# Performance work log

Hardware: AMD Instinct MI355X
Metric: run time of the kernel (lower is better)

Reference implementation:

```python
import jax, jax.numpy as jnp
import numpy as np

S = 3      # num_subset
CI = 64    # inter_channels
C = 256    # in_channels == out_channels
T = 400    # num_frame
V = 25     # num_node


def make_pe(channel, joint_num, time_len, domain):
    if domain == 'temporal':
        pos = np.repeat(np.arange(time_len), joint_num).astype(np.float32)
    else:
        pos = np.tile(np.arange(joint_num), time_len).astype(np.float32)
    pe = np.zeros((time_len * joint_num, channel), dtype=np.float32)
    div = np.exp(np.arange(0, channel, 2, dtype=np.float32) * (-np.log(10000.0) / channel))
    pe[:, 0::2] = np.sin(pos[:, None] * div[None, :])
    pe[:, 1::2] = np.cos(pos[:, None] * div[None, :])
    pe = pe.reshape(time_len, joint_num, channel).transpose(2, 0, 1)[None]  # (1,C,T,V)
    return jnp.asarray(pe)


def setup_inputs() -> dict:
    key = jax.random.key(0)
    ks = jax.random.split(key, 10)
    def w(k, shape):
        return jax.random.normal(k, shape, jnp.float32) * 0.02
    return {
        'x': jax.random.normal(ks[0], (4, C, T, V), jnp.float32),
        'x1': jax.random.normal(ks[1], (4, C, T, V), jnp.float32),
        'pe_s': make_pe(C, V, T, 'spatial'),
        'pe_t': make_pe(C, V, T, 'temporal'),
        'in_nets_W': w(ks[2], (2 * S * CI, C)), 'in_nets_b': jnp.zeros((2 * S * CI,), jnp.float32),
        'alphas': jnp.ones((1, S, 1, 1), jnp.float32),
        'attention0s': jnp.ones((1, S, V, V), jnp.float32) / V,
        'out_nets_W': w(ks[3], (C, S * C)), 'out_nets_b': jnp.zeros((C,), jnp.float32),
        'out_nets_g': jnp.ones((C,), jnp.float32), 'out_nets_beta': jnp.zeros((C,), jnp.float32),
        'ff_nets_W': w(ks[4], (C, C)), 'ff_nets_b': jnp.zeros((C,), jnp.float32),
        'ff_nets_g': jnp.ones((C,), jnp.float32), 'ff_nets_beta': jnp.zeros((C,), jnp.float32),
        'in_nett_W': w(ks[5], (2 * S * CI, C)), 'in_nett_b': jnp.zeros((2 * S * CI,), jnp.float32),
        'alphat': jnp.ones((1, S, 1, 1), jnp.float32),
        'attention0t': jnp.broadcast_to(jnp.eye(T, dtype=jnp.float32), (1, S, T, T)),
        'out_nett_W': w(ks[6], (C, S * C)), 'out_nett_b': jnp.zeros((C,), jnp.float32),
        'out_nett_g': jnp.ones((C,), jnp.float32), 'out_nett_beta': jnp.zeros((C,), jnp.float32),
        'ff_nett_W': w(ks[7], (C, C)), 'ff_nett_b': jnp.zeros((C,), jnp.float32),
        'ff_nett_g': jnp.ones((C,), jnp.float32), 'ff_nett_beta': jnp.zeros((C,), jnp.float32),
        'case': 0,
    }


def _conv1x1(W, b, x):
    return jnp.einsum('oc,nctv->notv', W, x) + b[None, :, None, None]

def _bn(x, g, b):  # eval-mode BN (running mean 0, var 1) -> channel affine
    return x * g[None, :, None, None] + b[None, :, None, None]

def _lrelu(x):
    return jnp.where(x >= 0, x, 0.1 * x)


def reference(x, x1, pe_s, pe_t, in_nets_W, in_nets_b, alphas, attention0s,
              out_nets_W, out_nets_b, out_nets_g, out_nets_beta,
              ff_nets_W, ff_nets_b, ff_nets_g, ff_nets_beta,
              in_nett_W, in_nett_b, alphat, attention0t,
              out_nett_W, out_nett_b, out_nett_g, out_nett_beta,
              ff_nett_W, ff_nett_b, ff_nett_g, ff_nett_beta, case):
    # case == 0 path of the original forward (dropout p=0 -> identity).
    def spatial(xi):
        y = xi + pe_s  # spatial positional encoding
        def half(xh, yh):  # xh, yh: (2, C, T, V) half-batch, as in x.view(2,2,C,T,V)
            qk = _conv1x1(in_nets_W, in_nets_b, yh).reshape(2, 2 * S, CI, T, V)
            q, k = qk[:, :S], qk[:, S:]
            att = jnp.tanh(jnp.einsum('nsctu,nsctv->nsuv', q, k) / (CI * T)) * alphas + attention0s
            return jnp.einsum('nctv,nsvw->nsctw', xh, att).reshape(2, S * C, T, V)
        z = jnp.concatenate([half(xi[:2], y[:2]), half(xi[2:], y[2:])], axis=0)
        h = _lrelu(xi + _bn(_conv1x1(out_nets_W, out_nets_b, z), out_nets_g, out_nets_beta))
        return _lrelu(xi + _bn(_conv1x1(ff_nets_W, ff_nets_b, h), ff_nets_g, ff_nets_beta))

    def temporal(yi):
        z = yi + pe_t  # temporal positional encoding
        def half(yh, zh):
            qk = _conv1x1(in_nett_W, in_nett_b, zh).reshape(2, 2 * S, CI, T, V)
            q, k = qk[:, :S], qk[:, S:]
            att = jnp.tanh(jnp.einsum('nsctv,nscqv->nstq', q, k) / (CI * V)) * alphat + attention0t
            return jnp.einsum('nctv,nstq->nscqv', yh, att).reshape(2, S * C, T, V)
        z2 = jnp.concatenate([half(yi[:2], z[:2]), half(yi[2:], z[2:])], axis=0)
        h = _lrelu(yi + _bn(_conv1x1(out_nett_W, out_nett_b, z2), out_nett_g, out_nett_beta))
        return _lrelu(yi + _bn(_conv1x1(ff_nett_W, ff_nett_b, h), ff_nett_g, ff_nett_beta))

    out0 = temporal(spatial(x))
    out1 = temporal(spatial(x1))
    return jnp.stack([out0, out1], axis=0)  # (2, 4, C, T, V)
```

## Files before the change

### kernel.cpp

```cpp
#include <hip/hip_runtime.h>
#include <math.h>


#define PP 10000
#define SAMP 2560000

typedef __attribute__((ext_vector_type(8))) __bf16 bf16x8;
typedef __attribute__((ext_vector_type(4))) float f32x4;

#define LIDX(g, r)  ((g) * 128 + ((r) ^ (g)))
#define LIDXB(g, r) ((g) * 64 + ((r) ^ (g)))

__device__ __forceinline__ float4 ld4(const float* p) { return *(const float4*)p; }
__device__ __forceinline__ float lrelu(float v) { return v >= 0.f ? v : 0.1f * v; }

template<int MODE, bool PE, bool BGLOB, bool OUTGLOB>
__global__ __launch_bounds__(256)
void gemm_mfma(const float* __restrict__ W, int Kw,
               const float* __restrict__ bias,
               const float* __restrict__ g, const float* __restrict__ beta,
               const float* __restrict__ bg0, const float* __restrict__ bg1,
               const float* __restrict__ bw,
               const float* __restrict__ pe,
               const float* rg0, const float* rg1,
               float* out, int n0, int M, int K)
{
    const int ln = blockIdx.z;
    const int ns = n0 + ln;
    const int p0 = blockIdx.x * 64;
    const int m0 = blockIdx.y * 128;
    const int tid = threadIdx.x;

    const float* Bp;
    if (BGLOB)
        Bp = (ns < 4) ? bg0 + (size_t)ns * (size_t)K * PP
                      : bg1 + (size_t)(ns - 4) * (size_t)K * PP;
    else
        Bp = bw + (size_t)ln * (size_t)K * PP;

    __shared__ __align__(16) bf16x8 AhL[512];
    __shared__ __align__(16) bf16x8 AlL[512];
    __shared__ __align__(16) bf16x8 BhL[256];
    __shared__ __align__(16) bf16x8 BlL[256];

    const int am  = tid >> 1;
    const int akb = (tid & 1) * 16;
    const int ag0 = akb >> 3;
    const float* wrow = W + (size_t)(m0 + am) * Kw + akb;

    const int bp  = tid & 63;
    const int bg_ = tid >> 6;
    const int bkg = bg_ * 8;
    const int gp  = p0 + bp;
    const bool pok = gp < PP;

    const int lane = tid & 63;
    const int wv = tid >> 6;
    const int wr = (wv >> 1) * 64, wc = (wv & 1) * 32;
    const int lr = lane & 15;
    const int lg = lane >> 4;

    f32x4 acc[4][2];
#pragma unroll
    for (int i = 0; i < 4; i++)
#pragma unroll
        for (int j = 0; j < 2; j++) acc[i][j] = (f32x4){0.f, 0.f, 0.f, 0.f};

    float4 wreg[4];
    float  breg[8];

    auto loadAB = [&](int kc) {
#pragma unroll
        for (int q = 0; q < 4; q++) wreg[q] = ld4(wrow + kc + q * 4);
        const int kk = kc + bkg;
#pragma unroll
        for (int i = 0; i < 8; i++) {
            float v = 0.f;
            if (pok) {
                v = Bp[(size_t)(kk + i) * PP + gp];
                if (PE) v += pe[(size_t)(kk + i) * PP + gp];
            }
            breg[i] = v;
        }
    };

    loadAB(0);

    for (int k0 = 0; k0 < K; k0 += 32) {
        {
            bf16x8 h0, h1, l0, l1;
#pragma unroll
            for (int q = 0; q < 4; q++) {
                const float vs0 = wreg[q].x, vs1 = wreg[q].y, vs2 = wreg[q].z, vs3 = wreg[q].w;
                __bf16 hh; const int ib = q * 4;
#define CVTA(c, val) { hh = (__bf16)(val); __bf16 ll = (__bf16)((val) - (float)hh); \
    if (ib + c < 8) { h0[ib + c] = hh; l0[ib + c] = ll; } else { h1[ib + c - 8] = hh; l1[ib + c - 8] = ll; } }
                CVTA(0, vs0) CVTA(1, vs1) CVTA(2, vs2) CVTA(3, vs3)
#undef CVTA
            }
            AhL[LIDX(ag0, am)]     = h0;
            AhL[LIDX(ag0 + 1, am)] = h1;
            AlL[LIDX(ag0, am)]     = l0;
            AlL[LIDX(ag0 + 1, am)] = l1;
        }
        {
            bf16x8 hb, lb;
#pragma unroll
            for (int i = 0; i < 8; i++) {
                __bf16 hh = (__bf16)breg[i];
                hb[i] = hh;
                lb[i] = (__bf16)(breg[i] - (float)hh);
            }
            BhL[LIDXB(bg_, bp)] = hb;
            BlL[LIDXB(bg_, bp)] = lb;
        }
        __syncthreads();

        const int kn = k0 + 32;
        if (kn < K) loadAB(kn);

        bf16x8 fbh[2], fbl[2];
#pragma unroll
        for (int fj = 0; fj < 2; fj++) {
            fbh[fj] = BhL[LIDXB(lg, wc + fj * 16 + lr)];
            fbl[fj] = BlL[LIDXB(lg, wc + fj * 16 + lr)];
        }
#pragma unroll
        for (int fi = 0; fi < 4; fi++) {
            bf16x8 fah = AhL[LIDX(lg, wr + fi * 16 + lr)];
            bf16x8 fal = AlL[LIDX(lg, wr + fi * 16 + lr)];
#pragma unroll
            for (int fj = 0; fj < 2; fj++) {
                acc[fi][fj] = __builtin_amdgcn_mfma_f32_16x16x32_bf16(fah, fbh[fj], acc[fi][fj], 0, 0, 0);
                acc[fi][fj] = __builtin_amdgcn_mfma_f32_16x16x32_bf16(fah, fbl[fj], acc[fi][fj], 0, 0, 0);
                acc[fi][fj] = __builtin_amdgcn_mfma_f32_16x16x32_bf16(fal, fbh[fj], acc[fi][fj], 0, 0, 0);
            }
        }
        __syncthreads();
    }

    const int rb = (lane >> 4) * 4;

    if (MODE == 5) {
#pragma unroll
        for (int fi = 0; fi < 4; fi++) {
            const int mb = m0 + wr + fi * 16 + rb;
            const int sec = mb >> 6, cl = mb & 63;
            float* qt = out + (size_t)ln * 3840000ull + (size_t)sec * 640000ull + cl;
            const float b0 = bias[mb], b1 = bias[mb + 1], b2 = bias[mb + 2], b3 = bias[mb + 3];
#pragma unroll
            for (int fj = 0; fj < 2; fj++) {
                const int p = p0 + wc + fj * 16 + lr;
                if (p >= PP) continue;
                const int t = p / 25, v = p - t * 25;
                f32x4 a = acc[fi][fj];
                *(float4*)(qt + (size_t)t * 1600 + v * 64) =
                    make_float4(a[0] + b0, a[1] + b1, a[2] + b2, a[3] + b3);
            }
        }
        return;
    }

    float* op = out + (OUTGLOB ? (size_t)ns : (size_t)ln) * (size_t)M * PP;
    const float* resp = nullptr;
    if (MODE == 1 || MODE == 4)
        resp = (ns < 4) ? rg0 + (size_t)ns * SAMP : rg1 + (size_t)(ns - 4) * SAMP;

#pragma unroll
    for (int fi = 0; fi < 4; fi++) {
#pragma unroll
        for (int r = 0; r < 4; r++) {
            const int m = m0 + wr + fi * 16 + rb + r;
            const float bi = (MODE == 0 || MODE == 1 || MODE == 4) ? bias[m] : 0.f;
            const float gi = (MODE == 1 || MODE == 4) ? g[m] : 0.f;
            const float be = (MODE == 1 || MODE == 4) ? beta[m] : 0.f;
            const size_t rowoff = (size_t)m * PP;
#pragma unroll
            for (int fj = 0; fj < 2; fj++) {
                const int p = p0 + wc + fj * 16 + lr;
                if (p >= PP) continue;
                const float a = acc[fi][fj][r];
                float val;
                if (MODE == 0)      val = a + bi;
                else if (MODE == 2) val = a;
                else if (MODE == 3) val = op[rowoff + p] + a;
                else if (MODE == 4) val = lrelu(resp[rowoff + p] + gi * (op[rowoff + p] + a + bi) + be);
                else                val = lrelu(resp[rowoff + p] + gi * (a + bi) + be);
                op[rowoff + p] = val;
            }
        }
    }
}

__global__ __launch_bounds__(256)
void apply_t_mfma(const float* __restrict__ y, const float* __restrict__ attT,
                  float* __restrict__ z, int n0, int s)
{
    const int ln = blockIdx.z;
    const int ns = n0 + ln;
    const int j0 = blockIdx.x * 64;
    const int q0 = blockIdx.y * 128;
    const float* A = attT + ((size_t)ln * 3 + s) * 160000ull;
    const float* Y = y + (size_t)ns * SAMP;
    float* zout = z + (size_t)ln * SAMP;
    const int tid = threadIdx.x;

    __shared__ __align__(16) bf16x8 AhL[512];
    __shared__ __align__(16) bf16x8 AlL[512];
    __shared__ __align__(16) bf16x8 BhL[256];
    __shared__ __align__(16) bf16x8 BlL[256];

    const int am  = tid >> 1;
    const int akb = (tid & 1) * 16;
    const int ag0 = akb >> 3;
    const int qA  = q0 + am;
    const float* arow = A + (size_t)qA * 400;

    const int bp  = tid & 63;
    const int bg_ = tid >> 6;
    const int bkg = bg_ * 8;
    const int j   = j0 + bp;
    const int cB  = j / 25, vB = j % 25;
    const float* yrow = Y + (size_t)cB * PP + vB;

    const int lane = tid & 63;
    const int wv = tid >> 6;
    const int wr = (wv >> 1) * 64, wc = (wv & 1) * 32;
    const int lr = lane & 15;
    const int lg = lane >> 4;

    f32x4 acc[4][2];
#pragma unroll
    for (int i = 0; i < 4; i++)
#pragma unroll
        for (int jj = 0; jj < 2; jj++) acc[i][jj] = (f32x4){0.f, 0.f, 0.f, 0.f};

    float4 wreg[4];
    float  breg[8];

    auto loadAB = [&](int kc) {
#pragma unroll
        for (int q = 0; q < 4; q++) {
            const int ks_ = kc + akb + q * 4;
            float4 v = make_float4(0.f, 0.f, 0.f, 0.f);
            if (qA < 400 && ks_ < 400) v = ld4(arow + ks_);
            wreg[q] = v;
        }
        const int kb = kc + bkg;
#pragma unroll
        for (int i = 0; i < 8; i++) {
            const int t = kb + i;
            breg[i] = (t < 400) ? yrow[(size_t)t * 25] : 0.f;
        }
    };

    loadAB(0);

    for (int k0 = 0; k0 < 416; k0 += 32) {
        {
            bf16x8 h0, h1, l0, l1;
#pragma unroll
            for (int q = 0; q < 4; q++) {
                const float vs0 = wreg[q].x, vs1 = wreg[q].y, vs2 = wreg[q].z, vs3 = wreg[q].w;
                __bf16 hh; const int ib = q * 4;
#define CVTA(c, val) { hh = (__bf16)(val); __bf16 ll = (__bf16)((val) - (float)hh); \
    if (ib + c < 8) { h0[ib + c] = hh; l0[ib + c] = ll; } else { h1[ib + c - 8] = hh; l1[ib + c - 8] = ll; } }
                CVTA(0, vs0) CVTA(1, vs1) CVTA(2, vs2) CVTA(3, vs3)
#undef CVTA
            }
            AhL[LIDX(ag0, am)]     = h0;
            AhL[LIDX(ag0 + 1, am)] = h1;
            AlL[LIDX(ag0, am)]     = l0;
            AlL[LIDX(ag0 + 1, am)] = l1;
        }
        {
            bf16x8 hb, lb;
#pragma unroll
            for (int i = 0; i < 8; i++) {
                __bf16 hh = (__bf16)breg[i];
                hb[i] = hh;
                lb[i] = (__bf16)(breg[i] - (float)hh);
            }
            BhL[LIDXB(bg_, bp)] = hb;
            BlL[LIDXB(bg_, bp)] = lb;
        }
        __syncthreads();

        const int kn = k0 + 32;
        if (kn < 416) loadAB(kn);

        bf16x8 fbh[2], fbl[2];
#pragma unroll
        for (int fj = 0; fj < 2; fj++) {
            fbh[fj] = BhL[LIDXB(lg, wc + fj * 16 + lr)];
            fbl[fj] = BlL[LIDXB(lg, wc + fj * 16 + lr)];
        }
#pragma unroll
        for (int fi = 0; fi < 4; fi++) {
            bf16x8 fah = AhL[LIDX(lg, wr + fi * 16 + lr)];
            bf16x8 fal = AlL[LIDX(lg, wr + fi * 16 + lr)];
#pragma unroll
            for (int fj = 0; fj < 2; fj++) {
                acc[fi][fj] = __builtin_amdgcn_mfma_f32_16x16x32_bf16(fah, fbh[fj], acc[fi][fj], 0, 0, 0);
                acc[fi][fj] = __builtin_amdgcn_mfma_f32_16x16x32_bf16(fah, fbl[fj], acc[fi][fj], 0, 0, 0);
                acc[fi][fj] = __builtin_amdgcn_mfma_f32_16x16x32_bf16(fal, fbh[fj], acc[fi][fj], 0, 0, 0);
            }
        }
        __syncthreads();
    }

    const int rb = (lane >> 4) * 4;
#pragma unroll
    for (int fi = 0; fi < 4; fi++) {
#pragma unroll
        for (int r = 0; r < 4; r++) {
            const int q = q0 + wr + fi * 16 + rb + r;
            if (q >= 400) continue;
#pragma unroll
            for (int fj = 0; fj < 2; fj++) {
                const int p = j0 + wc + fj * 16 + lr;
                const int c = p / 25, v = p - c * 25;
                zout[(size_t)c * PP + (size_t)q * 25 + v] = acc[fi][fj][r];
            }
        }
    }
}

__global__ __launch_bounds__(256)
void scores_t_mfma(const float* __restrict__ qkT,
                   const float* __restrict__ alphat,
                   const float* __restrict__ att0t,
                   float* __restrict__ aT)
{
    const int idx = blockIdx.y;
    const int s = idx % 3, ln = idx / 3;
    const int t0 = (blockIdx.x % 7) * 64;
    const int q0 = (blockIdx.x / 7) * 128;
    const float* base = qkT + (size_t)ln * 3840000ull;
    const float* Aq = base + (size_t)(3 + s) * 640000ull;
    const float* Bt = base + (size_t)s * 640000ull;
    const int tid = threadIdx.x;

    __shared__ __align__(16) bf16x8 AhL[512];
    __shared__ __align__(16) bf16x8 AlL[512];
    __shared__ __align__(16) bf16x8 BhL[256];
    __shared__ __align__(16) bf16x8 BlL[256];

    const int am  = tid >> 1;
    const int akb = (tid & 1) * 16;
    const int ag0 = akb >> 3;
    const int qA  = q0 + am;
    const float* arow = Aq + (size_t)qA * 1600 + akb;
    const bool aok = qA < 400;

    const int bp  = tid & 63;
    const int bg_ = tid >> 6;
    const int bkg = bg_ * 8;
    const int tB  = t0 + bp;
    const float* brow = Bt + (size_t)tB * 1600 + bkg;
    const bool bok = tB < 400;

    const int lane = tid & 63;
    const int wv = tid >> 6;
    const int wr = (wv >> 1) * 64, wc = (wv & 1) * 32;
    const int lr = lane & 15;
    const int lg = lane >> 4;

    f32x4 acc[4][2];
#pragma unroll
    for (int i = 0; i < 4; i++)
#pragma unroll
        for (int j = 0; j < 2; j++) acc[i][j] = (f32x4){0.f, 0.f, 0.f, 0.f};

    float4 areg[4];
    float4 brg[2];

    auto loadAB = [&](int kc) {
#pragma unroll
        for (int q = 0; q < 4; q++)
            areg[q] = aok ? ld4(arow + kc + q * 4) : make_float4(0.f, 0.f, 0.f, 0.f);
        brg[0] = bok ? ld4(brow + kc)     : make_float4(0.f, 0.f, 0.f, 0.f);
        brg[1] = bok ? ld4(brow + kc + 4) : make_float4(0.f, 0.f, 0.f, 0.f);
    };

    loadAB(0);

    for (int k0 = 0; k0 < 1600; k0 += 32) {
        {
            bf16x8 h0, h1, l0, l1;
#pragma unroll
            for (int q = 0; q < 4; q++) {
                const float vs0 = areg[q].x, vs1 = areg[q].y, vs2 = areg[q].z, vs3 = areg[q].w;
                __bf16 hh; const int ib = q * 4;
#define CVTA(c, val) { hh = (__bf16)(val); __bf16 ll = (__bf16)((val) - (float)hh); \
    if (ib + c < 8) { h0[ib + c] = hh; l0[ib + c] = ll; } else { h1[ib + c - 8] = hh; l1[ib + c - 8] = ll; } }
                CVTA(0, vs0) CVTA(1, vs1) CVTA(2, vs2) CVTA(3, vs3)
#undef CVTA
            }
            AhL[LIDX(ag0, am)]     = h0;
            AhL[LIDX(ag0 + 1, am)] = h1;
            AlL[LIDX(ag0, am)]     = l0;
            AlL[LIDX(ag0 + 1, am)] = l1;
        }
        {
            bf16x8 hb, lb;
#pragma unroll
            for (int e = 0; e < 2; e++) {
                const float v0 = (e ? brg[1].x : brg[0].x), v1 = (e ? brg[1].y : brg[0].y);
                const float v2 = (e ? brg[1].z : brg[0].z), v3 = (e ? brg[1].w : brg[0].w);
                __bf16 hh;
#define CVTB(c, val) { hh = (__bf16)(val); hb[e * 4 + c] = hh; lb[e * 4 + c] = (__bf16)((val) - (float)hh); }
                CVTB(0, v0) CVTB(1, v1) CVTB(2, v2) CVTB(3, v3)
#undef CVTB
            }
            BhL[LIDXB(bg_, bp)] = hb;
            BlL[LIDXB(bg_, bp)] = lb;
        }
        __syncthreads();

        const int kn = k0 + 32;
        if (kn < 1600) loadAB(kn);

        bf16x8 fbh[2], fbl[2];
#pragma unroll
        for (int fj = 0; fj < 2; fj++) {
            fbh[fj] = BhL[LIDXB(lg, wc + fj * 16 + lr)];
            fbl[fj] = BlL[LIDXB(lg, wc + fj * 16 + lr)];
        }
#pragma unroll
        for (int fi = 0; fi < 4; fi++) {
            bf16x8 fah = AhL[LIDX(lg, wr + fi * 16 + lr)];
            bf16x8 fal = AlL[LIDX(lg, wr + fi * 16 + lr)];
#pragma unroll
            for (int fj = 0; fj < 2; fj++) {
                acc[fi][fj] = __builtin_amdgcn_mfma_f32_16x16x32_bf16(fah, fbh[fj], acc[fi][fj], 0, 0, 0);
                acc[fi][fj] = __builtin_amdgcn_mfma_f32_16x16x32_bf16(fah, fbl[fj], acc[fi][fj], 0, 0, 0);
                acc[fi][fj] = __builtin_amdgcn_mfma_f32_16x16x32_bf16(fal, fbh[fj], acc[fi][fj], 0, 0, 0);
            }
        }
        __syncthreads();
    }

    const int rb = (lane >> 4) * 4;
    const float al = alphat[s];
    float* aTp = aT + (size_t)idx * 160000ull;
    const float* a0p = att0t + (size_t)s * 160000ull;

#pragma unroll
    for (int fi = 0; fi < 4; fi++) {
        const int qb = q0 + wr + fi * 16 + rb;
#pragma unroll
        for (int fj = 0; fj < 2; fj++) {
            const int t = t0 + wc + fj * 16 + lr;
            if (t >= 400) continue;
#pragma unroll
            for (int r = 0; r < 4; r++) {
                const int q = qb + r;
                if (q >= 400) continue;
                aTp[(size_t)q * 400 + t] =
                    tanhf(acc[fi][fj][r] * (1.f / 1600.f)) * al + a0p[(size_t)t * 400 + q];
            }
        }
    }
}

__global__ __launch_bounds__(256)
void scores_s_partial(const float* __restrict__ qk, float* __restrict__ part)
{
    const int chunk = blockIdx.x, s = blockIdx.y, ln = blockIdx.z;
    const float* qsec = qk + ((size_t)ln * 384 + s * 64) * PP + (size_t)chunk * 3200;
    const float* ksec = qk + ((size_t)ln * 384 + (3 + s) * 64) * PP + (size_t)chunk * 3200;
    __shared__ float QL[3200];
    __shared__ float KL[3200];
    const int tid = threadIdx.x;
    for (int i = tid; i < 3200; i += 256) {
        QL[i] = qsec[i];
        KL[i] = ksec[i];
    }
    __syncthreads();
    const int o0 = tid, o1 = tid + 256, o2 = tid + 512;
    const int u0 = o0 / 25, v0 = o0 % 25;
    const int u1 = o1 / 25, v1 = o1 % 25;
    const int u2 = o2 / 25, v2 = o2 % 25;
    float a0 = 0.f, a1 = 0.f, a2 = 0.f;
#pragma unroll 8
    for (int r = 0; r < 128; r++) {
        int ro = r * 25;
        a0 = fmaf(QL[ro + u0], KL[ro + v0], a0);
        a1 = fmaf(QL[ro + u1], KL[ro + v1], a1);
        if (tid < 113) a2 = fmaf(QL[ro + u2], KL[ro + v2], a2);
    }
    float* pp = part + (((size_t)(ln * 3 + s)) * 200 + chunk) * 625;
    pp[o0] = a0;
    pp[o1] = a1;
    if (tid < 113) pp[o2] = a2;
}

__global__ void scores_s_final(const float* __restrict__ part,
                               const float* __restrict__ alphas,
                               const float* __restrict__ att0s,
                               float* __restrict__ atts)
{
    const int idx = blockIdx.x;
    const int s = idx % 3;
    const int o = threadIdx.x;
    if (o >= 625) return;
    const float* pb = part + (size_t)idx * 200 * 625 + o;
    float sum = 0.f;
#pragma unroll 8
    for (int i = 0; i < 200; i++) sum += pb[(size_t)i * 625];
    atts[(size_t)idx * 625 + o] = tanhf(sum * (1.f / 25600.f)) * alphas[s] + att0s[s * 625 + o];
}

__global__ __launch_bounds__(256)
void apply_s_kernel(const float* __restrict__ x0, const float* __restrict__ x1,
                    const float* __restrict__ atts, float* __restrict__ z,
                    int n0, int s)
{
    const int ln = blockIdx.y;
    const int ns = n0 + ln;
    const int tid = threadIdx.x;
    __shared__ float attL[700];
    for (int i = tid; i < 700; i += 256) attL[i] = 0.f;
    __syncthreads();
    for (int i = tid; i < 625; i += 256) {
        int v = i / 25, w = i % 25;
        attL[v * 28 + w] = atts[(size_t)ln * 1875 + s * 625 + i];
    }
    __syncthreads();
    const float* xp = (ns < 4) ? x0 + (size_t)ns * SAMP : x1 + (size_t)(ns - 4) * SAMP;
    const int r0 = (blockIdx.x * 256 + tid) * 2;
    const float* xr0 = xp + (size_t)r0 * 25;
    float xr[2][25];
#pragma unroll
    for (int i = 0; i < 2; i++)
#pragma unroll
        for (int v = 0; v < 25; v++) xr[i][v] = xr0[i * 25 + v];
    const int c0 = r0 / 400, t0 = r0 % 400;

    float4 acc0[7], acc1[7];
#pragma unroll
    for (int w4 = 0; w4 < 7; w4++) {
        acc0[w4] = make_float4(0.f, 0.f, 0.f, 0.f);
        acc1[w4] = make_float4(0.f, 0.f, 0.f, 0.f);
    }
#pragma unroll
    for (int v = 0; v < 25; v++) {
        const float4* arow = (const float4*)&attL[v * 28];
        float xv0 = xr[0][v], xv1 = xr[1][v];
#pragma unroll
        for (int w4 = 0; w4 < 7; w4++) {
            float4 a = arow[w4];
            acc0[w4].x = fmaf(xv0, a.x, acc0[w4].x);
            acc0[w4].y = fmaf(xv0, a.y, acc0[w4].y);
            acc0[w4].z = fmaf(xv0, a.z, acc0[w4].z);
            acc0[w4].w = fmaf(xv0, a.w, acc0[w4].w);
            acc1[w4].x = fmaf(xv1, a.x, acc1[w4].x);
            acc1[w4].y = fmaf(xv1, a.y, acc1[w4].y);
            acc1[w4].z = fmaf(xv1, a.z, acc1[w4].z);
            acc1[w4].w = fmaf(xv1, a.w, acc1[w4].w);
        }
    }
    float* zp = z + (size_t)ln * SAMP + (size_t)c0 * PP + (size_t)t0 * 25;
#pragma unroll
    for (int w4 = 0; w4 < 7; w4++) {
        int wb = w4 * 4;
        if (wb + 0 < 25) zp[wb + 0] = acc0[w4].x;
        if (wb + 1 < 25) zp[wb + 1] = acc0[w4].y;
        if (wb + 2 < 25) zp[wb + 2] = acc0[w4].z;
        if (wb + 3 < 25) zp[wb + 3] = acc0[w4].w;
    }
#pragma unroll
    for (int w4 = 0; w4 < 7; w4++) {
        int wb = w4 * 4;
        if (wb + 0 < 25) zp[25 + wb + 0] = acc1[w4].x;
        if (wb + 1 < 25) zp[25 + wb + 1] = acc1[w4].y;
        if (wb + 2 < 25) zp[25 + wb + 2] = acc1[w4].z;
        if (wb + 3 < 25) zp[25 + wb + 3] = acc1[w4].w;
    }
}

extern "C" void kernel_launch(void* const* d_in, const int* in_sizes, int n_in,
                              void* d_out, int out_size, void* d_ws, size_t ws_size,
                              hipStream_t stream)
{
    const float* x    = (const float*)d_in[0];
    const float* x1   = (const float*)d_in[1];
    const float* pe_s = (const float*)d_in[2];
    const float* pe_t = (const float*)d_in[3];
    const float* Wsi  = (const float*)d_in[4];
    const float* bsi  = (const float*)d_in[5];
    const float* alphas = (const float*)d_in[6];
    const float* att0s  = (const float*)d_in[7];
    const float* Wso  = (const float*)d_in[8];
    const float* bso  = (const float*)d_in[9];
    const float* gso  = (const float*)d_in[10];
    const float* beso = (const float*)d_in[11];
    const float* Wsf  = (const float*)d_in[12];
    const float* bsf  = (const float*)d_in[13];
    const float* gsf  = (const float*)d_in[14];
    const float* besf = (const float*)d_in[15];
    const float* Wti  = (const float*)d_in[16];
    const float* bti  = (const float*)d_in[17];
    const float* alphat = (const float*)d_in[18];
    const float* att0t  = (const float*)d_in[19];
    const float* Wto  = (const float*)d_in[20];
    const float* bto  = (const float*)d_in[21];
    const float* gto  = (const float*)d_in[22];
    const float* beto = (const float*)d_in[23];
    const float* Wtf  = (const float*)d_in[24];
    const float* btf  = (const float*)d_in[25];
    const float* gtf  = (const float*)d_in[26];
    const float* betf = (const float*)d_in[27];

    float* outp = (float*)d_out;
    const float* outpB = outp + 4ull * SAMP;

    int G = 1;
    for (int g = 8; g >= 1; g >>= 1) {
        if ((size_t)g * 27587500ull <= ws_size) { G = g; break; }
    }

    float* A   = (float*)d_ws;
    float* Zs  = A  + (size_t)G * 3840000ull;
    float* aT  = Zs + (size_t)G * 2560000ull;
    float* sp  = aT + (size_t)G * 480000ull;
    float* as  = sp + (size_t)G * 15000ull;

    dim3 blk(256);
    for (int n0 = 0; n0 < 8; n0 += G) {
        dim3 gIn(157, 3, G), gOut(157, 2, G);

        gemm_mfma<0, true, true, false><<<gIn, blk, 0, stream>>>(
            Wsi, 256, bsi, nullptr, nullptr, x, x1, nullptr, pe_s,
            nullptr, nullptr, A, n0, 384, 256);
        scores_s_partial<<<dim3(200, 3, G), blk, 0, stream>>>(A, Zs);
        scores_s_final<<<dim3(3 * G), dim3(640), 0, stream>>>(Zs, alphas, att0s, as);
        for (int s = 0; s < 3; s++) {
            apply_s_kernel<<<dim3(200, G), blk, 0, stream>>>(x, x1, as, Zs, n0, s);
            if (s == 0)
                gemm_mfma<2, false, false, false><<<gOut, blk, 0, stream>>>(
                    Wso + s * 256, 768, nullptr, nullptr, nullptr, nullptr, nullptr, Zs,
                    nullptr, nullptr, nullptr, A, n0, 256, 256);
            else if (s == 1)
                gemm_mfma<3, false, false, false><<<gOut, blk, 0, stream>>>(
                    Wso + s * 256, 768, nullptr, nullptr, nullptr, nullptr, nullptr, Zs,
                    nullptr, nullptr, nullptr, A, n0, 256, 256);
            else
                gemm_mfma<4, false, false, false><<<gOut, blk, 0, stream>>>(
                    Wso + s * 256, 768, bso, gso, beso, nullptr, nullptr, Zs,
                    nullptr, x, x1, A, n0, 256, 256);
        }
        gemm_mfma<1, false, false, true><<<gOut, blk, 0, stream>>>(
            Wsf, 256, bsf, gsf, besf, nullptr, nullptr, A, nullptr,
            x, x1, outp, n0, 256, 256);

        gemm_mfma<5, true, true, false><<<gIn, blk, 0, stream>>>(
            Wti, 256, bti, nullptr, nullptr, outp, outpB, nullptr, pe_t,
            nullptr, nullptr, A, n0, 384, 256);
        scores_t_mfma<<<dim3(28, 3 * G), blk, 0, stream>>>(A, alphat, att0t, aT);
        for (int s = 0; s < 3; s++) {
            apply_t_mfma<<<dim3(100, 4, G), blk, 0, stream>>>(outp, aT, Zs, n0, s);
            if (s == 0)
                gemm_mfma<2, false, false, false><<<gOut, blk, 0, stream>>>(
                    Wto + s * 256, 768, nullptr, nullptr, nullptr, nullptr, nullptr, Zs,
                    nullptr, nullptr, nullptr, A, n0, 256, 256);
            else if (s == 1)
                gemm_mfma<3, false, false, false><<<gOut, blk, 0, stream>>>(
                    Wto + s * 256, 768, nullptr, nullptr, nullptr, nullptr, nullptr, Zs,
                    nullptr, nullptr, nullptr, A, n0, 256, 256);
            else
                gemm_mfma<4, false, false, false><<<gOut, blk, 0, stream>>>(
                    Wto + s * 256, 768, bto, gto, beto, nullptr, nullptr, Zs,
                    nullptr, outp, outpB, A, n0, 256, 256);
        }
        gemm_mfma<1, false, false, true><<<gOut, blk, 0, stream>>>(
            Wtf, 256, btf, gtf, betf, nullptr, nullptr, A, nullptr,
            outp, outpB, outp, n0, 256, 256);
    }
}
```

Baseline: 1.812 ms.

## Merge per-subset output GEMMs into one K=768 GEMM over stacked Z buffers

Apply kernels now write each subset's result into its own slice of a tripled Z workspace. A single output-projection GEMM with K=768 then runs with the fused BN/residual/lrelu epilogue. This replaces three K=256 GEMMs that read-modify-wrote partial sums through global memory. The cost is a larger workspace per sample, which may reduce the batch group size G if the workspace is limited.

```diff
diff --git a/kernel.cpp b/kernel.cpp
--- a/kernel.cpp
+++ b/kernel.cpp
@@ -163,7 +163,7 @@
 
     float* op = out + (OUTGLOB ? (size_t)ns : (size_t)ln) * (size_t)M * PP;
     const float* resp = nullptr;
-    if (MODE == 1 || MODE == 4)
+    if (MODE == 1)
         resp = (ns < 4) ? rg0 + (size_t)ns * SAMP : rg1 + (size_t)(ns - 4) * SAMP;
 
 #pragma unroll
@@ -171,9 +171,9 @@
 #pragma unroll
         for (int r = 0; r < 4; r++) {
             const int m = m0 + wr + fi * 16 + rb + r;
-            const float bi = (MODE == 0 || MODE == 1 || MODE == 4) ? bias[m] : 0.f;
-            const float gi = (MODE == 1 || MODE == 4) ? g[m] : 0.f;
-            const float be = (MODE == 1 || MODE == 4) ? beta[m] : 0.f;
+            const float bi = (MODE == 0 || MODE == 1) ? bias[m] : 0.f;
+            const float gi = (MODE == 1) ? g[m] : 0.f;
+            const float be = (MODE == 1) ? beta[m] : 0.f;
             const size_t rowoff = (size_t)m * PP;
 #pragma unroll
             for (int fj = 0; fj < 2; fj++) {
@@ -181,11 +181,8 @@
                 if (p >= PP) continue;
                 const float a = acc[fi][fj][r];
                 float val;
-                if (MODE == 0)      val = a + bi;
-                else if (MODE == 2) val = a;
-                else if (MODE == 3) val = op[rowoff + p] + a;
-                else if (MODE == 4) val = lrelu(resp[rowoff + p] + gi * (op[rowoff + p] + a + bi) + be);
-                else                val = lrelu(resp[rowoff + p] + gi * (a + bi) + be);
+                if (MODE == 0) val = a + bi;
+                else           val = lrelu(resp[rowoff + p] + gi * (a + bi) + be);
                 op[rowoff + p] = val;
             }
         }
@@ -202,7 +199,7 @@
     const int q0 = blockIdx.y * 128;
     const float* A = attT + ((size_t)ln * 3 + s) * 160000ull;
     const float* Y = y + (size_t)ns * SAMP;
-    float* zout = z + (size_t)ln * SAMP;
+    float* zout = z + ((size_t)ln * 3 + s) * SAMP;
     const int tid = threadIdx.x;
 
     __shared__ __align__(16) bf16x8 AhL[512];
@@ -561,7 +558,7 @@
             acc1[w4].w = fmaf(xv1, a.w, acc1[w4].w);
         }
     }
-    float* zp = z + (size_t)ln * SAMP + (size_t)c0 * PP + (size_t)t0 * 25;
+    float* zp = z + ((size_t)ln * 3 + s) * SAMP + (size_t)c0 * PP + (size_t)t0 * 25;
 #pragma unroll
     for (int w4 = 0; w4 < 7; w4++) {
         int wb = w4 * 4;
@@ -618,14 +615,13 @@
 
     int G = 1;
     for (int g = 8; g >= 1; g >>= 1) {
-        if ((size_t)g * 27587500ull <= ws_size) { G = g; break; }
+        if ((size_t)g * 48007500ull <= ws_size) { G = g; break; }
     }
 
     float* A   = (float*)d_ws;
     float* Zs  = A  + (size_t)G * 3840000ull;
-    float* aT  = Zs + (size_t)G * 2560000ull;
-    float* sp  = aT + (size_t)G * 480000ull;
-    float* as  = sp + (size_t)G * 15000ull;
+    float* aT  = Zs + (size_t)G * 7680000ull;
+    float* as  = aT + (size_t)G * 480000ull;
 
     dim3 blk(256);
     for (int n0 = 0; n0 < 8; n0 += G) {
@@ -636,21 +632,11 @@
             nullptr, nullptr, A, n0, 384, 256);
         scores_s_partial<<<dim3(200, 3, G), blk, 0, stream>>>(A, Zs);
         scores_s_final<<<dim3(3 * G), dim3(640), 0, stream>>>(Zs, alphas, att0s, as);
-        for (int s = 0; s < 3; s++) {
+        for (int s = 0; s < 3; s++)
             apply_s_kernel<<<dim3(200, G), blk, 0, stream>>>(x, x1, as, Zs, n0, s);
-            if (s == 0)
-                gemm_mfma<2, false, false, false><<<gOut, blk, 0, stream>>>(
-                    Wso + s * 256, 768, nullptr, nullptr, nullptr, nullptr, nullptr, Zs,
-                    nullptr, nullptr, nullptr, A, n0, 256, 256);
-            else if (s == 1)
-                gemm_mfma<3, false, false, false><<<gOut, blk, 0, stream>>>(
-                    Wso + s * 256, 768, nullptr, nullptr, nullptr, nullptr, nullptr, Zs,
-                    nullptr, nullptr, nullptr, A, n0, 256, 256);
-            else
-                gemm_mfma<4, false, false, false><<<gOut, blk, 0, stream>>>(
-                    Wso + s * 256, 768, bso, gso, beso, nullptr, nullptr, Zs,
-                    nullptr, x, x1, A, n0, 256, 256);
-        }
+        gemm_mfma<1, false, false, false><<<gOut, blk, 0, stream>>>(
+            Wso, 768, bso, gso, beso, nullptr, nullptr, Zs,
+            nullptr, x, x1, A, n0, 256, 768);
         gemm_mfma<1, false, false, true><<<gOut, blk, 0, stream>>>(
             Wsf, 256, bsf, gsf, besf, nullptr, nullptr, A, nullptr,
             x, x1, outp, n0, 256, 256);
@@ -659,21 +645,11 @@
             Wti, 256, bti, nullptr, nullptr, outp, outpB, nullptr, pe_t,
             nullptr, nullptr, A, n0, 384, 256);
         scores_t_mfma<<<dim3(28, 3 * G), blk, 0, stream>>>(A, alphat, att0t, aT);
-        for (int s = 0; s < 3; s++) {
+        for (int s = 0; s < 3; s++)
             apply_t_mfma<<<dim3(100, 4, G), blk, 0, stream>>>(outp, aT, Zs, n0, s);
-            if (s == 0)
-                gemm_mfma<2, false, false, false><<<gOut, blk, 0, stream>>>(
-                    Wto + s * 256, 768, nullptr, nullptr, nullptr, nullptr, nullptr, Zs,
-                    nullptr, nullptr, nullptr, A, n0, 256, 256);
-            else if (s == 1)
-                gemm_mfma<3, false, false, false><<<gOut, blk, 0, stream>>>(
-                    Wto + s * 256, 768, nullptr, nullptr, nullptr, nullptr, nullptr, Zs,
-                    nullptr, nullptr, nullptr, A, n0, 256, 256);
-            else
-                gemm_mfma<4, false, false, false><<<gOut, blk, 0, stream>>>(
-                    Wto + s * 256, 768, bto, gto, beto, nullptr, nullptr, Zs,
-                    nullptr, outp, outpB, A, n0, 256, 256);
-        }
+        gemm_mfma<1, false, false, false><<<gOut, blk, 0, stream>>>(
+            Wto, 768, bto, gto, beto, nullptr, nullptr, Zs,
+            nullptr, outp, outpB, A, n0, 256, 768);
         gemm_mfma<1, false, false, true><<<gOut, blk, 0, stream>>>(
             Wtf, 256, btf, gtf, betf, nullptr, nullptr, A, nullptr,
             outp, outpB, outp, n0, 256, 256);
```

Result: slower. 1.903 ms (+5.0%).
